# Optimization experiments

Hardware: AMD Instinct MI355X
Metric: run time of the kernel (lower is better)

Reference implementation:

```python
import jax, jax.numpy as jnp
import numpy as np

N = 50000      # nodes
E = 800000     # edges (before self-loops)
IN = 128       # in_channels
HID = 32       # hidden_channels
H = 4          # num_heads
OUT = 2        # out_channels
NEG_SLOPE = 0.2


def setup_inputs() -> dict:
    key = jax.random.key(0)
    ks = jax.random.split(key, 16)
    s = 0.1
    x = jax.random.normal(ks[0], (N, IN), jnp.float32)
    edge_index = jax.random.randint(ks[1], (2, E), 0, N, dtype=jnp.int32)
    W1 = jax.random.normal(ks[2], (IN, H * HID), jnp.float32) * s
    att_src1 = jax.random.normal(ks[3], (H, HID), jnp.float32) * s
    att_dst1 = jax.random.normal(ks[4], (H, HID), jnp.float32) * s
    b1 = jnp.zeros((H * HID,), jnp.float32)
    W2 = jax.random.normal(ks[5], (H * HID, H * HID), jnp.float32) * s
    att_src2 = jax.random.normal(ks[6], (H, HID), jnp.float32) * s
    att_dst2 = jax.random.normal(ks[7], (H, HID), jnp.float32) * s
    b2 = jnp.zeros((H * HID,), jnp.float32)
    W3 = jax.random.normal(ks[8], (H * HID, OUT), jnp.float32) * s
    att_src3 = jax.random.normal(ks[9], (1, OUT), jnp.float32) * s
    att_dst3 = jax.random.normal(ks[10], (1, OUT), jnp.float32) * s
    b3 = jnp.zeros((OUT,), jnp.float32)
    return {"x": x, "edge_index": edge_index,
            "W1": W1, "att_src1": att_src1, "att_dst1": att_dst1, "b1": b1,
            "W2": W2, "att_src2": att_src2, "att_dst2": att_dst2, "b2": b2,
            "W3": W3, "att_src3": att_src3, "att_dst3": att_dst3, "b3": b3}


def gat_layer(x, src, dst, W, a_src, a_dst, b, heads, ch, concat):
    """PyG GATConv (eval mode): per-edge LeakyReLU attention, edge-softmax over
    incoming edges of each destination node, weighted scatter-add aggregation."""
    n = x.shape[0]
    h = (x @ W).reshape(n, heads, ch)                      # [N,H,C]
    alpha_s = jnp.sum(h * a_src, axis=-1)                  # [N,H]
    alpha_d = jnp.sum(h * a_dst, axis=-1)                  # [N,H]
    alpha = jax.nn.leaky_relu(alpha_s[src] + alpha_d[dst], NEG_SLOPE)  # [E',H]
    amax = jax.ops.segment_max(alpha, dst, num_segments=n)             # [N,H]
    e = jnp.exp(alpha - amax[dst])
    denom = jax.ops.segment_sum(e, dst, num_segments=n)
    w = e / denom[dst]                                     # softmax weights [E',H]
    out = jax.ops.segment_sum(h[src] * w[:, :, None], dst, num_segments=n)  # [N,H,C]
    out = out.reshape(n, heads * ch) if concat else out.mean(axis=1)
    return out + b


def reference(x, edge_index, W1, att_src1, att_dst1, b1,
              W2, att_src2, att_dst2, b2, W3, att_src3, att_dst3, b3):
    # PyG GATConv adds self-loops by default
    loop = jnp.arange(N, dtype=edge_index.dtype)
    src = jnp.concatenate([edge_index[0], loop])
    dst = jnp.concatenate([edge_index[1], loop])
    h = jax.nn.elu(gat_layer(x, src, dst, W1, att_src1, att_dst1, b1, H, HID, True))
    h = jax.nn.elu(gat_layer(h, src, dst, W2, att_src2, att_dst2, b2, H, HID, True))
    h = gat_layer(h, src, dst, W3, att_src3, att_dst3, b3, 1, OUT, False)
    return jax.nn.log_softmax(h, axis=1)
```

## Files before the change

### kernel.cpp

```cpp
#include <hip/hip_runtime.h>
#include <hip/hip_fp16.h>

#define NN 50000
#define EE 800000
#define ET 850000
#define NEG 0.2f
#define SCAN_B 1024
#define NBLK ((NN + SCAN_B - 1) / SCAN_B)

__device__ __forceinline__ float leaky(float x) { return fmaxf(x, NEG * x); }
__device__ __forceinline__ float elu_f(float x) { return x > 0.f ? x : expm1f(x); }

struct alignas(8) half4 { __half2 a, b; };

__global__ void hist_k(const int* __restrict__ ei, int* __restrict__ counts) {
    int i = blockIdx.x * blockDim.x + threadIdx.x;
    if (i >= ET) return;
    int dst = (i < EE) ? ei[EE + i] : (i - EE);
    atomicAdd(&counts[dst], 1);
}

__global__ void scan1_k(const int* __restrict__ counts, int* __restrict__ rp,
                        int* __restrict__ bsums) {
    __shared__ int lsum[256];
    int base = blockIdx.x * SCAN_B;
    int v[4];
    int tsum = 0;
#pragma unroll
    for (int j = 0; j < 4; ++j) {
        int i = base + threadIdx.x * 4 + j;
        v[j] = (i < NN) ? counts[i] : 0;
        tsum += v[j];
    }
    lsum[threadIdx.x] = tsum;
    __syncthreads();
    for (int off = 1; off < 256; off <<= 1) {
        int t = (threadIdx.x >= off) ? lsum[threadIdx.x - off] : 0;
        __syncthreads();
        lsum[threadIdx.x] += t;
        __syncthreads();
    }
    int excl = lsum[threadIdx.x] - tsum;
#pragma unroll
    for (int j = 0; j < 4; ++j) {
        int i = base + threadIdx.x * 4 + j;
        if (i < NN) rp[i] = excl;
        excl += v[j];
    }
    if (threadIdx.x == 255) bsums[blockIdx.x] = lsum[255];
}

__global__ void scan2_k(int* __restrict__ bsums, int* __restrict__ rp) {
    int lane = threadIdx.x;
    int v = (lane < NBLK) ? bsums[lane] : 0;
    int orig = v;
    for (int off = 1; off < 64; off <<= 1) {
        int t = __shfl_up(v, off, 64);
        if (lane >= off) v += t;
    }
    if (lane < NBLK) bsums[lane] = v - orig;
    if (lane == 63) rp[NN] = v;
}

__global__ void scan3_k(int* __restrict__ rp, const int* __restrict__ bsums) {
    int add = bsums[blockIdx.x];
    int base = blockIdx.x * SCAN_B + threadIdx.x * 4;
#pragma unroll
    for (int j = 0; j < 4; ++j) {
        int i = base + j;
        if (i < NN) rp[i] += add;
    }
}

__global__ void scatter_k(const int* __restrict__ ei, const int* __restrict__ rp,
                          int* __restrict__ fill, int* __restrict__ csr) {
    int i = blockIdx.x * blockDim.x + threadIdx.x;
    if (i >= ET) return;
    int src, dst;
    if (i < EE) { src = ei[i]; dst = ei[EE + i]; }
    else        { src = dst = i - EE; }
    int pos = rp[dst] + atomicAdd(&fill[dst], 1);
    csr[pos] = src;
}

__global__ __launch_bounds__(256, 2)
void gemm128_k(const float* __restrict__ X, const float* __restrict__ W,
               __half* __restrict__ Yh, int nrows,
               const float* __restrict__ att_s, const float* __restrict__ att_d,
               float* __restrict__ asb, float* __restrict__ adb) {
    __shared__ __align__(16) float Wl[128 * 128];
    __shared__ __align__(16) float Xs[32 * 128];
    for (int i = threadIdx.x; i < 128 * 128 / 4; i += 256)
        ((float4*)Wl)[i] = ((const float4*)W)[i];

    int tc = threadIdx.x & 31;
    int tr = threadIdx.x >> 5;
    float4 avs = ((const float4*)att_s)[tc];
    float4 avd = ((const float4*)att_d)[tc];

    for (int row0 = blockIdx.x * 32; row0 < nrows; row0 += gridDim.x * 32) {
        __syncthreads();
        for (int i = threadIdx.x; i < 32 * 128 / 4; i += 256) {
            int r = i >> 5, c4 = i & 31;
            int row = row0 + r;
            float4 v = (row < nrows) ? ((const float4*)(X + (size_t)row * 128))[c4]
                                     : make_float4(0.f, 0.f, 0.f, 0.f);
            ((float4*)Xs)[i] = v;
        }
        __syncthreads();

        float acc[4][4] = {};
        for (int k = 0; k < 128; k += 4) {
            float4 w0 = ((float4*)(Wl + (k + 0) * 128))[tc];
            float4 w1 = ((float4*)(Wl + (k + 1) * 128))[tc];
            float4 w2 = ((float4*)(Wl + (k + 2) * 128))[tc];
            float4 w3 = ((float4*)(Wl + (k + 3) * 128))[tc];
#pragma unroll
            for (int r = 0; r < 4; ++r) {
                float4 xv = *((float4*)(Xs + (tr * 4 + r) * 128 + k));
                acc[r][0] += xv.x * w0.x + xv.y * w1.x + xv.z * w2.x + xv.w * w3.x;
                acc[r][1] += xv.x * w0.y + xv.y * w1.y + xv.z * w2.y + xv.w * w3.y;
                acc[r][2] += xv.x * w0.z + xv.y * w1.z + xv.z * w2.z + xv.w * w3.z;
                acc[r][3] += xv.x * w0.w + xv.y * w1.w + xv.z * w2.w + xv.w * w3.w;
            }
        }
#pragma unroll
        for (int r = 0; r < 4; ++r) {
            int row = row0 + tr * 4 + r;
            if (row < nrows) {
                half4 hv;
                hv.a = __floats2half2_rn(acc[r][0], acc[r][1]);
                hv.b = __floats2half2_rn(acc[r][2], acc[r][3]);
                ((half4*)(Yh + (size_t)row * 128))[tc] = hv;
            }
        }

        __syncthreads();
        float* red = Xs;
#pragma unroll
        for (int r = 0; r < 4; ++r) {
            int rl = tr * 4 + r;
            float ps = acc[r][0]*avs.x + acc[r][1]*avs.y + acc[r][2]*avs.z + acc[r][3]*avs.w;
            float pd = acc[r][0]*avd.x + acc[r][1]*avd.y + acc[r][2]*avd.z + acc[r][3]*avd.w;
            red[(0*32 + rl)*33 + tc] = ps;
            red[(1*32 + rl)*33 + tc] = pd;
        }
        __syncthreads();
        {
            int rl = threadIdx.x & 31;
            int j  = threadIdx.x >> 5;
            int head = j >> 1, sd = j & 1;
            float sum = 0.f;
#pragma unroll
            for (int q = 0; q < 8; ++q)
                sum += red[(sd*32 + rl)*33 + head*8 + q];
            int row = row0 + rl;
            if (row < nrows) (sd ? adb : asb)[row*4 + head] = sum;
        }
    }
}

__global__ __launch_bounds__(256)
void agg_k(const __half* __restrict__ Hh, const float* __restrict__ asb,
           const float* __restrict__ adb, const int* __restrict__ rp,
           const int* __restrict__ csr, const float* __restrict__ bias,
           float* __restrict__ Y,
           const float* __restrict__ W3, const float* __restrict__ s3w,
           const float* __restrict__ d3w, float* __restrict__ h3,
           float* __restrict__ as3, float* __restrict__ ad3) {
    int lane = threadIdx.x & 63;
    int hw = lane >> 5;
    int l  = lane & 31;
    int n = blockIdx.x * 8 + (threadIdx.x >> 6) * 2 + hw;
    if (n >= NN) return;
    int hd = l >> 3;
    float ad = adb[n * 4 + hd];
    float acc0 = 0.f, acc1 = 0.f, acc2 = 0.f, acc3 = 0.f, den = 0.f;
    int e = rp[n], end = rp[n + 1], last = end - 1;
    for (int base = e; base < end; base += 8) {
        int s[8]; float a[8]; float2 hraw[8];
#pragma unroll
        for (int j = 0; j < 8; ++j) {
            int i = base + j;
            s[j] = csr[i <= last ? i : last];
        }
#pragma unroll
        for (int j = 0; j < 8; ++j) a[j] = asb[s[j] * 4 + hd] + ad;
#pragma unroll
        for (int j = 0; j < 8; ++j)
            hraw[j] = ((const float2*)(Hh + (size_t)s[j] * 128))[l];
#pragma unroll
        for (int j = 0; j < 8; ++j) {
            float w = __expf(leaky(a[j]));
            w = (base + j <= last) ? w : 0.f;
            den += w;
            const __half2* hp = (const __half2*)&hraw[j];
            float2 f01 = __half22float2(hp[0]);
            float2 f23 = __half22float2(hp[1]);
            acc0 += w * f01.x; acc1 += w * f01.y;
            acc2 += w * f23.x; acc3 += w * f23.y;
        }
    }
    float4 bv = ((const float4*)bias)[l];
    float inv = 1.f / den;
    float o0 = elu_f(acc0 * inv + bv.x);
    float o1 = elu_f(acc1 * inv + bv.y);
    float o2 = elu_f(acc2 * inv + bv.z);
    float o3 = elu_f(acc3 * inv + bv.w);
    if (!W3) {
        ((float4*)(Y + (size_t)n * 128))[l] = make_float4(o0, o1, o2, o3);
    } else {
        float4 wa = ((const float4*)W3)[l * 2];
        float4 wb = ((const float4*)W3)[l * 2 + 1];
        float p0 = o0 * wa.x + o1 * wa.z + o2 * wb.x + o3 * wb.z;
        float p1 = o0 * wa.y + o1 * wa.w + o2 * wb.y + o3 * wb.w;
        for (int off = 16; off > 0; off >>= 1) {
            p0 += __shfl_down(p0, off, 32);
            p1 += __shfl_down(p1, off, 32);
        }
        if (l == 0) {
            h3[n * 2 + 0] = p0;
            h3[n * 2 + 1] = p1;
            as3[n] = p0 * s3w[0] + p1 * s3w[1];
            ad3[n] = p0 * d3w[0] + p1 * d3w[1];
        }
    }
}

__global__ void l3agg_k(const float* __restrict__ h3, const float* __restrict__ as3,
                        const float* __restrict__ ad3, const int* __restrict__ rp,
                        const int* __restrict__ csr, const float* __restrict__ b3,
                        float* __restrict__ out) {
    int n = blockIdx.x * blockDim.x + threadIdx.x;
    if (n >= NN) return;
    const float2* h2 = (const float2*)h3;
    float adn = ad3[n];
    float den = 0.f, a0 = 0.f, a1 = 0.f;
    int e = rp[n], end = rp[n + 1], last = end - 1;
    for (int base = e; base < end; base += 4) {
        int s[4]; float al[4]; float2 g[4];
#pragma unroll
        for (int j = 0; j < 4; ++j) {
            int i = base + j;
            s[j] = csr[i <= last ? i : last];
        }
#pragma unroll
        for (int j = 0; j < 4; ++j) al[j] = as3[s[j]] + adn;
#pragma unroll
        for (int j = 0; j < 4; ++j) g[j] = h2[s[j]];
#pragma unroll
        for (int j = 0; j < 4; ++j) {
            float w = __expf(leaky(al[j]));
            w = (base + j <= last) ? w : 0.f;
            den += w;
            a0 += w * g[j].x;
            a1 += w * g[j].y;
        }
    }
    float o0 = a0 / den + b3[0];
    float o1 = a1 / den + b3[1];
    float m = fmaxf(o0, o1);
    float lse = m + logf(__expf(o0 - m) + __expf(o1 - m));
    out[n * 2 + 0] = o0 - lse;
    out[n * 2 + 1] = o1 - lse;
}

extern "C" void kernel_launch(void* const* d_in, const int* in_sizes, int n_in,
                              void* d_out, int out_size, void* d_ws, size_t ws_size,
                              hipStream_t stream) {
    const float* x   = (const float*)d_in[0];
    const int*   ei  = (const int*)d_in[1];
    const float* W1  = (const float*)d_in[2];
    const float* as1 = (const float*)d_in[3];
    const float* ad1 = (const float*)d_in[4];
    const float* b1  = (const float*)d_in[5];
    const float* W2  = (const float*)d_in[6];
    const float* as2 = (const float*)d_in[7];
    const float* ad2 = (const float*)d_in[8];
    const float* b2  = (const float*)d_in[9];
    const float* W3  = (const float*)d_in[10];
    const float* s3w = (const float*)d_in[11];
    const float* d3w = (const float*)d_in[12];
    const float* b3  = (const float*)d_in[13];
    float* out = (float*)d_out;

    char* ws = (char*)d_ws;
    size_t off = 0;
    auto alloc = [&](size_t bytes) -> char* {
        char* p = ws + off;
        off = (off + bytes + 255) & ~(size_t)255;
        return p;
    };
    __half* hA    = (__half*)alloc((size_t)NN * 128 * 2);
    float* hB     = (float*)alloc((size_t)NN * 128 * 4);
    float* asb    = (float*)alloc((size_t)NN * 4 * 4);
    float* adb    = (float*)alloc((size_t)NN * 4 * 4);
    int*   rp     = (int*)alloc((size_t)(NN + 1) * 4);
    int*   counts = (int*)alloc((size_t)NN * 4);
    int*   csr    = (int*)alloc((size_t)ET * 4);
    int*   bsums  = (int*)alloc((size_t)NBLK * 4);
    float* h3     = (float*)alloc((size_t)NN * 2 * 4);
    float* s3     = (float*)alloc((size_t)NN * 4);
    float* d3     = (float*)alloc((size_t)NN * 4);

    hipMemsetAsync(counts, 0, (size_t)NN * 4, stream);
    hist_k<<<(ET + 255) / 256, 256, 0, stream>>>(ei, counts);
    scan1_k<<<NBLK, 256, 0, stream>>>(counts, rp, bsums);
    scan2_k<<<1, 64, 0, stream>>>(bsums, rp);
    scan3_k<<<NBLK, 256, 0, stream>>>(rp, bsums);
    hipMemsetAsync(counts, 0, (size_t)NN * 4, stream);
    scatter_k<<<(ET + 255) / 256, 256, 0, stream>>>(ei, rp, counts, csr);

    gemm128_k<<<512, 256, 0, stream>>>(x, W1, hA, NN, as1, ad1, asb, adb);
    agg_k<<<(NN + 7) / 8, 256, 0, stream>>>(hA, asb, adb, rp, csr, b1, hB,
                                            nullptr, nullptr, nullptr,
                                            nullptr, nullptr, nullptr);

    gemm128_k<<<512, 256, 0, stream>>>(hB, W2, hA, NN, as2, ad2, asb, adb);
    agg_k<<<(NN + 7) / 8, 256, 0, stream>>>(hA, asb, adb, rp, csr, b2, nullptr,
                                            W3, s3w, d3w, h3, s3, d3);

    l3agg_k<<<(NN + 255) / 256, 256, 0, stream>>>(h3, s3, d3, rp, csr, b3, out);
}
```

Measured before the change: 332.9 us.

## Use MFMA fp16 GEMM, store layer-1 output in half, reuse hist ranks for CSR

Replaces the shared-memory FP32 SIMT GEMM with a wave-level MFMA 16x16x32 fp16 kernel that reads a pre-transposed half-precision weight matrix and computes the attention dot products with lane shuffles. The layer-1 aggregation now writes its activations in fp16, which halves the intermediate traffic and feeds the second GEMM directly. The histogram kernel records each edge's atomic rank, so CSR scatter no longer needs a second memset and atomic pass. These changes reduce compute and memory cost, but add fp16 rounding of the inputs and weights, two small transpose kernels, and an extra rank buffer.

```diff
diff --git a/kernel.cpp b/kernel.cpp
--- a/kernel.cpp
+++ b/kernel.cpp
@@ -13,11 +13,15 @@
 
 struct alignas(8) half4 { __half2 a, b; };
 
-__global__ void hist_k(const int* __restrict__ ei, int* __restrict__ counts) {
+typedef _Float16 half8_t __attribute__((ext_vector_type(8)));
+typedef float float4_t __attribute__((ext_vector_type(4)));
+
+__global__ void hist_k(const int* __restrict__ ei, int* __restrict__ counts,
+                       int* __restrict__ rank) {
     int i = blockIdx.x * blockDim.x + threadIdx.x;
     if (i >= ET) return;
     int dst = (i < EE) ? ei[EE + i] : (i - EE);
-    atomicAdd(&counts[dst], 1);
+    rank[i] = atomicAdd(&counts[dst], 1);
 }
 
 __global__ void scan1_k(const int* __restrict__ counts, int* __restrict__ rp,
@@ -73,89 +77,89 @@
 }
 
 __global__ void scatter_k(const int* __restrict__ ei, const int* __restrict__ rp,
-                          int* __restrict__ fill, int* __restrict__ csr) {
+                          const int* __restrict__ rank, int* __restrict__ csr) {
     int i = blockIdx.x * blockDim.x + threadIdx.x;
     if (i >= ET) return;
     int src, dst;
     if (i < EE) { src = ei[i]; dst = ei[EE + i]; }
     else        { src = dst = i - EE; }
-    int pos = rp[dst] + atomicAdd(&fill[dst], 1);
-    csr[pos] = src;
-}
-
-__global__ __launch_bounds__(256, 2)
-void gemm128_k(const float* __restrict__ X, const float* __restrict__ W,
-               __half* __restrict__ Yh, int nrows,
-               const float* __restrict__ att_s, const float* __restrict__ att_d,
-               float* __restrict__ asb, float* __restrict__ adb) {
-    __shared__ __align__(16) float Wl[128 * 128];
-    __shared__ __align__(16) float Xs[32 * 128];
-    for (int i = threadIdx.x; i < 128 * 128 / 4; i += 256)
-        ((float4*)Wl)[i] = ((const float4*)W)[i];
-
-    int tc = threadIdx.x & 31;
-    int tr = threadIdx.x >> 5;
-    float4 avs = ((const float4*)att_s)[tc];
-    float4 avd = ((const float4*)att_d)[tc];
-
-    for (int row0 = blockIdx.x * 32; row0 < nrows; row0 += gridDim.x * 32) {
-        __syncthreads();
-        for (int i = threadIdx.x; i < 32 * 128 / 4; i += 256) {
-            int r = i >> 5, c4 = i & 31;
-            int row = row0 + r;
-            float4 v = (row < nrows) ? ((const float4*)(X + (size_t)row * 128))[c4]
-                                     : make_float4(0.f, 0.f, 0.f, 0.f);
-            ((float4*)Xs)[i] = v;
-        }
-        __syncthreads();
-
-        float acc[4][4] = {};
-        for (int k = 0; k < 128; k += 4) {
-            float4 w0 = ((float4*)(Wl + (k + 0) * 128))[tc];
-            float4 w1 = ((float4*)(Wl + (k + 1) * 128))[tc];
-            float4 w2 = ((float4*)(Wl + (k + 2) * 128))[tc];
-            float4 w3 = ((float4*)(Wl + (k + 3) * 128))[tc];
-#pragma unroll
-            for (int r = 0; r < 4; ++r) {
-                float4 xv = *((float4*)(Xs + (tr * 4 + r) * 128 + k));
-                acc[r][0] += xv.x * w0.x + xv.y * w1.x + xv.z * w2.x + xv.w * w3.x;
-                acc[r][1] += xv.x * w0.y + xv.y * w1.y + xv.z * w2.y + xv.w * w3.y;
-                acc[r][2] += xv.x * w0.z + xv.y * w1.z + xv.z * w2.z + xv.w * w3.z;
-                acc[r][3] += xv.x * w0.w + xv.y * w1.w + xv.z * w2.w + xv.w * w3.w;
-            }
-        }
-#pragma unroll
-        for (int r = 0; r < 4; ++r) {
-            int row = row0 + tr * 4 + r;
+    csr[rp[dst] + rank[i]] = src;
+}
+
+__global__ void wt_k(const float* __restrict__ W, __half* __restrict__ Wt) {
+    int i = blockIdx.x * 256 + threadIdx.x;
+    int k = i >> 7, n = i & 127;
+    Wt[n * 128 + k] = __float2half(W[i]);
+}
+
+__global__ __launch_bounds__(256)
+void gemm_mfma_k(const float* __restrict__ Xf, const __half* __restrict__ Xh,
+                 const __half* __restrict__ Wt, __half* __restrict__ Yh, int nrows,
+                 const float* __restrict__ att_s, const float* __restrict__ att_d,
+                 float* __restrict__ asb, float* __restrict__ adb) {
+    int lane = threadIdx.x & 63;
+    int wid  = threadIdx.x >> 6;
+    int n = lane & 15, quad = lane >> 4;
+    float atts_r[8], attd_r[8];
+#pragma unroll
+    for (int t = 0; t < 8; ++t) {
+        atts_r[t] = att_s[t * 16 + n];
+        attd_r[t] = att_d[t * 16 + n];
+    }
+    for (int row0 = (blockIdx.x * 4 + wid) * 16; row0 < nrows; row0 += gridDim.x * 64) {
+        float4_t acc[8];
+#pragma unroll
+        for (int t = 0; t < 8; ++t) acc[t] = (float4_t){0.f, 0.f, 0.f, 0.f};
+        int rA = row0 + n; if (rA >= nrows) rA = nrows - 1;
+#pragma unroll
+        for (int ch = 0; ch < 4; ++ch) {
+            half8_t a;
+            if (Xh) {
+                a = *(const half8_t*)(Xh + (size_t)rA * 128 + ch * 32 + quad * 8);
+            } else {
+                const float* xp = Xf + (size_t)rA * 128 + ch * 32 + quad * 8;
+                float4 f0 = *(const float4*)xp;
+                float4 f1 = *(const float4*)(xp + 4);
+                a = (half8_t){(_Float16)f0.x, (_Float16)f0.y, (_Float16)f0.z, (_Float16)f0.w,
+                              (_Float16)f1.x, (_Float16)f1.y, (_Float16)f1.z, (_Float16)f1.w};
+            }
+#pragma unroll
+            for (int t = 0; t < 8; ++t) {
+                half8_t b = *(const half8_t*)(Wt + (t * 16 + n) * 128 + ch * 32 + quad * 8);
+                acc[t] = __builtin_amdgcn_mfma_f32_16x16x32_f16(a, b, acc[t], 0, 0, 0);
+            }
+        }
+#pragma unroll
+        for (int rg = 0; rg < 4; ++rg) {
+            int row = row0 + quad * 4 + rg;
             if (row < nrows) {
-                half4 hv;
-                hv.a = __floats2half2_rn(acc[r][0], acc[r][1]);
-                hv.b = __floats2half2_rn(acc[r][2], acc[r][3]);
-                ((half4*)(Yh + (size_t)row * 128))[tc] = hv;
-            }
-        }
-
-        __syncthreads();
-        float* red = Xs;
-#pragma unroll
-        for (int r = 0; r < 4; ++r) {
-            int rl = tr * 4 + r;
-            float ps = acc[r][0]*avs.x + acc[r][1]*avs.y + acc[r][2]*avs.z + acc[r][3]*avs.w;
-            float pd = acc[r][0]*avd.x + acc[r][1]*avd.y + acc[r][2]*avd.z + acc[r][3]*avd.w;
-            red[(0*32 + rl)*33 + tc] = ps;
-            red[(1*32 + rl)*33 + tc] = pd;
-        }
-        __syncthreads();
-        {
-            int rl = threadIdx.x & 31;
-            int j  = threadIdx.x >> 5;
-            int head = j >> 1, sd = j & 1;
-            float sum = 0.f;
-#pragma unroll
-            for (int q = 0; q < 8; ++q)
-                sum += red[(sd*32 + rl)*33 + head*8 + q];
-            int row = row0 + rl;
-            if (row < nrows) (sd ? adb : asb)[row*4 + head] = sum;
+                __half* yp = Yh + (size_t)row * 128 + n;
+#pragma unroll
+                for (int t = 0; t < 8; ++t)
+                    yp[t * 16] = __float2half(acc[t][rg]);
+            }
+        }
+#pragma unroll
+        for (int rg = 0; rg < 4; ++rg) {
+            float ps[4], pd[4];
+#pragma unroll
+            for (int h = 0; h < 4; ++h) {
+                ps[h] = acc[2*h][rg] * atts_r[2*h] + acc[2*h+1][rg] * atts_r[2*h+1];
+                pd[h] = acc[2*h][rg] * attd_r[2*h] + acc[2*h+1][rg] * attd_r[2*h+1];
+#pragma unroll
+                for (int mask = 1; mask < 16; mask <<= 1) {
+                    ps[h] += __shfl_xor(ps[h], mask, 64);
+                    pd[h] += __shfl_xor(pd[h], mask, 64);
+                }
+            }
+            int row = row0 + quad * 4 + rg;
+            if (n == 0 && row < nrows) {
+#pragma unroll
+                for (int h = 0; h < 4; ++h) {
+                    asb[row * 4 + h] = ps[h];
+                    adb[row * 4 + h] = pd[h];
+                }
+            }
         }
     }
 }
@@ -164,7 +168,7 @@
 void agg_k(const __half* __restrict__ Hh, const float* __restrict__ asb,
            const float* __restrict__ adb, const int* __restrict__ rp,
            const int* __restrict__ csr, const float* __restrict__ bias,
-           float* __restrict__ Y,
+           __half* __restrict__ Y,
            const float* __restrict__ W3, const float* __restrict__ s3w,
            const float* __restrict__ d3w, float* __restrict__ h3,
            float* __restrict__ as3, float* __restrict__ ad3) {
@@ -208,7 +212,10 @@
     float o2 = elu_f(acc2 * inv + bv.z);
     float o3 = elu_f(acc3 * inv + bv.w);
     if (!W3) {
-        ((float4*)(Y + (size_t)n * 128))[l] = make_float4(o0, o1, o2, o3);
+        half4 hv;
+        hv.a = __floats2half2_rn(o0, o1);
+        hv.b = __floats2half2_rn(o2, o3);
+        ((half4*)(Y + (size_t)n * 128))[l] = hv;
     } else {
         float4 wa = ((const float4*)W3)[l * 2];
         float4 wb = ((const float4*)W3)[l * 2 + 1];
@@ -292,31 +299,38 @@
         return p;
     };
     __half* hA    = (__half*)alloc((size_t)NN * 128 * 2);
-    float* hB     = (float*)alloc((size_t)NN * 128 * 4);
+    __half* hBh   = (__half*)alloc((size_t)NN * 128 * 2);
     float* asb    = (float*)alloc((size_t)NN * 4 * 4);
     float* adb    = (float*)alloc((size_t)NN * 4 * 4);
     int*   rp     = (int*)alloc((size_t)(NN + 1) * 4);
     int*   counts = (int*)alloc((size_t)NN * 4);
     int*   csr    = (int*)alloc((size_t)ET * 4);
+    int*   rank   = (int*)alloc((size_t)ET * 4);
     int*   bsums  = (int*)alloc((size_t)NBLK * 4);
+    __half* Wt1   = (__half*)alloc(128 * 128 * 2);
+    __half* Wt2   = (__half*)alloc(128 * 128 * 2);
     float* h3     = (float*)alloc((size_t)NN * 2 * 4);
     float* s3     = (float*)alloc((size_t)NN * 4);
     float* d3     = (float*)alloc((size_t)NN * 4);
 
+    wt_k<<<64, 256, 0, stream>>>(W1, Wt1);
+    wt_k<<<64, 256, 0, stream>>>(W2, Wt2);
+
     hipMemsetAsync(counts, 0, (size_t)NN * 4, stream);
-    hist_k<<<(ET + 255) / 256, 256, 0, stream>>>(ei, counts);
+    hist_k<<<(ET + 255) / 256, 256, 0, stream>>>(ei, counts, rank);
     scan1_k<<<NBLK, 256, 0, stream>>>(counts, rp, bsums);
     scan2_k<<<1, 64, 0, stream>>>(bsums, rp);
     scan3_k<<<NBLK, 256, 0, stream>>>(rp, bsums);
-    hipMemsetAsync(counts, 0, (size_t)NN * 4, stream);
-    scatter_k<<<(ET + 255) / 256, 256, 0, stream>>>(ei, rp, counts, csr);
-
-    gemm128_k<<<512, 256, 0, stream>>>(x, W1, hA, NN, as1, ad1, asb, adb);
-    agg_k<<<(NN + 7) / 8, 256, 0, stream>>>(hA, asb, adb, rp, csr, b1, hB,
+    scatter_k<<<(ET + 255) / 256, 256, 0, stream>>>(ei, rp, rank, csr);
+
+    gemm_mfma_k<<<(NN + 63) / 64, 256, 0, stream>>>(x, nullptr, Wt1, hA, NN,
+                                                    as1, ad1, asb, adb);
+    agg_k<<<(NN + 7) / 8, 256, 0, stream>>>(hA, asb, adb, rp, csr, b1, hBh,
                                             nullptr, nullptr, nullptr,
                                             nullptr, nullptr, nullptr);
 
-    gemm128_k<<<512, 256, 0, stream>>>(hB, W2, hA, NN, as2, ad2, asb, adb);
+    gemm_mfma_k<<<(NN + 63) / 64, 256, 0, stream>>>(nullptr, hBh, Wt2, hA, NN,
+                                                    as2, ad2, asb, adb);
     agg_k<<<(NN + 7) / 8, 256, 0, stream>>>(hA, asb, adb, rp, csr, b2, nullptr,
                                             W3, s3w, d3w, h3, s3, d3);
 
```

Result: faster. 290.6 us (-12.7%).
